# Optimization experiments

Hardware: AMD Instinct MI355X
Metric: run time of the kernel (lower is better)

Reference implementation:

```python
import jax, jax.numpy as jnp
import numpy as np

N, D, K = 32768, 256, 8192
SQRT3 = 3.0 ** 0.5


def setup_inputs() -> dict:
    key = jax.random.key(0)
    k1, k2 = jax.random.split(key)
    x = jax.random.normal(k1, (N, D), dtype=jnp.float32)
    # torch .uniform_(-sqrt(3), sqrt(3)) on an [D, K] table
    embeddings = jax.random.uniform(k2, (D, K), dtype=jnp.float32,
                                    minval=-SQRT3, maxval=SQRT3)
    return {"x": x, "embeddings": embeddings}


def reference(x, embeddings):
    # x: [N, D] (forward flattens from dim 1; 2D input is identity)
    # embeddings: [D, K]
    # squared L2 distances: ||y||^2 - 2 y.E + ||e||^2  -> [N, K]
    dist = (jnp.sum(x * x, axis=1, keepdims=True)
            - 2.0 * (x @ embeddings)
            + jnp.sum(embeddings * embeddings, axis=0, keepdims=True))
    idx = jnp.argmin(dist, axis=1)  # [N]
    # one_hot(idx) @ E^T == gather of columns of E (same math, no dense one-hot)
    quantized = jnp.take(embeddings, idx, axis=1).T  # [N, D]
    return quantized.reshape(x.shape)
```

## Files before the change

kernel.cpp:

```cpp
#include <hip/hip_runtime.h>
#include <math.h>
#include <float.h>

#define N_ROWS 32768
#define D_DIM  256
#define K_DIM  8192

#define EPS1 0.25f
#define EPS2 0.02f
#define T2CAP 4096
#define NSPLIT2 32
#define T3CAP 512
#define NSPLIT3 16

typedef _Float16 f16;
typedef _Float16 f16x8 __attribute__((ext_vector_type(8)));
typedef float f32x4 __attribute__((ext_vector_type(4)));
typedef unsigned long long u64;

#define KSPLIT 8
#define COLS_PER_SPLIT (K_DIM / KSPLIT)
#define CHUNK_COLS 32
#define NCHUNK (COLS_PER_SPLIT / CHUNK_COLS)
#define CHUNK_BYTES (CHUNK_COLS * D_DIM * 2)

#define NB_CONV 4096
#define NB_PREPE 512
#define NB_NHEN 32

typedef unsigned int u32;
typedef const u32 __attribute__((address_space(1)))* gas1_u32;
typedef u32 __attribute__((address_space(3)))* las3_u32;
__device__ __forceinline__ void gload_lds16(const void* g, void* l) {
    __builtin_amdgcn_global_load_lds((gas1_u32)g, (las3_u32)l, 16, 0, 0);
}

__global__ void prep_kernel(const float* __restrict__ X, const float* __restrict__ E,
                            f16* __restrict__ X16, float* __restrict__ ET,
                            f16* __restrict__ Epack, float* __restrict__ nhen,
                            int* __restrict__ count, int* __restrict__ count3) {
    __shared__ float t[64][65];
    const int bid = blockIdx.x;
    if (bid < NB_CONV) {
        if (bid == 0 && threadIdx.x == 0) { *count = 0; *count3 = 0; }
        const size_t i = ((size_t)bid * 256 + threadIdx.x) * 8;
        float4 a = *reinterpret_cast<const float4*>(X + i);
        float4 b = *reinterpret_cast<const float4*>(X + i + 4);
        f16x8 o;
        o[0]=(f16)a.x; o[1]=(f16)a.y; o[2]=(f16)a.z; o[3]=(f16)a.w;
        o[4]=(f16)b.x; o[5]=(f16)b.y; o[6]=(f16)b.z; o[7]=(f16)b.w;
        *reinterpret_cast<f16x8*>(X16 + i) = o;
    } else if (bid < NB_CONV + NB_PREPE) {
        const int pb = bid - NB_CONV;
        const int bk = pb & (K_DIM / 64 - 1);
        const int bd = pb >> 7;
        const int c  = threadIdx.x & 63;
        const int r0 = (threadIdx.x >> 6) * 16;
        const int d0 = bd * 64, k0 = bk * 64;
#pragma unroll
        for (int i = 0; i < 16; ++i)
            t[r0 + i][c] = E[(size_t)(d0 + r0 + i) * K_DIM + k0 + c];
        __syncthreads();
#pragma unroll
        for (int i = 0; i < 16; ++i)
            ET[(size_t)(k0 + r0 + i) * D_DIM + d0 + c] = t[c][r0 + i];
#pragma unroll
        for (int o = 0; o < 2; ++o) {
            const int out = threadIdx.x + o * 256;
            const int i16 = out >> 7;
            const int th  = (out >> 6) & 1;
            const int l   = out & 63;
            const int tile = bk * 4 + i16;
            const int tg   = bd * 2 + th;
            f16x8 frag;
#pragma unroll
            for (int j = 0; j < 8; ++j)
                frag[j] = (f16)t[32*th + (l >> 4) * 8 + j][16*i16 + (l & 15)];
            *reinterpret_cast<f16x8*>(Epack + ((size_t)(tile*8 + tg) * 512 + l * 8)) = frag;
        }
    } else {
        const int k = (bid - NB_CONV - NB_PREPE) * 256 + threadIdx.x;
        float s = 0.0f;
#pragma unroll 8
        for (int d = 0; d < D_DIM; ++d) {
            float v = E[(size_t)d * K_DIM + k];
            s = fmaf(v, v, s);
        }
        nhen[k] = -0.5f * s;
    }
}

__global__ void convx_kernel(const float* __restrict__ X, f16* __restrict__ X16,
                             int* __restrict__ count, int* __restrict__ count3) {
    if (blockIdx.x == 0 && threadIdx.x == 0) { *count = 0; *count3 = 0; }
    const size_t i = ((size_t)blockIdx.x * 256 + threadIdx.x) * 8;
    float4 a = *reinterpret_cast<const float4*>(X + i);
    float4 b = *reinterpret_cast<const float4*>(X + i + 4);
    f16x8 o;
    o[0]=(f16)a.x; o[1]=(f16)a.y; o[2]=(f16)a.z; o[3]=(f16)a.w;
    o[4]=(f16)b.x; o[5]=(f16)b.y; o[6]=(f16)b.z; o[7]=(f16)b.w;
    *reinterpret_cast<f16x8*>(X16 + i) = o;
}

__global__ void packe_kernel(const float* __restrict__ E, f16* __restrict__ Epack) {
    const int gid = blockIdx.x * 256 + threadIdx.x;
    const int l    = gid & 63;
    const int t    = (gid >> 6) & 7;
    const int tile = gid >> 9;
    const int k  = 16 * tile + (l & 15);
    const int d0 = 32 * t + (l >> 4) * 8;
    f16x8 o;
#pragma unroll
    for (int j = 0; j < 8; ++j) o[j] = (f16)E[(size_t)(d0 + j) * K_DIM + k];
    *reinterpret_cast<f16x8*>(Epack + (size_t)gid * 8) = o;
}

__global__ void nhen_kernel(const float* __restrict__ E, float* __restrict__ nhen) {
    const int k = blockIdx.x * 256 + threadIdx.x;
    float s = 0.0f;
#pragma unroll 8
    for (int d = 0; d < D_DIM; ++d) {
        float v = E[(size_t)d * K_DIM + k];
        s = fmaf(v, v, s);
    }
    nhen[k] = -0.5f * s;
}

__launch_bounds__(256, 2)
__global__ void pass1_kernel(const f16* __restrict__ X16,
                             const f16* __restrict__ Epack,
                             const float* __restrict__ nhen,
                             float* __restrict__ p_best,
                             float* __restrict__ p_sec,
                             int*   __restrict__ p_idx) {
    __shared__ f16 B_lds[3][CHUNK_BYTES / 2];
    __shared__ float nh_lds[COLS_PER_SPLIT];

    const int tid = threadIdx.x;
    const int wv = tid >> 6;
    const int lane = tid & 63;
    const int l15 = lane & 15;
    const int l4  = lane >> 4;
    const int rg = blockIdx.x >> 3;
    const int ks = blockIdx.x & 7;
    const int rowW = rg * 256 + wv * 64;
    const int colBase = ks * COLS_PER_SPLIT;

    f16x8 A[4][8];
#pragma unroll
    for (int rt = 0; rt < 4; ++rt)
#pragma unroll
        for (int t = 0; t < 8; ++t)
            A[rt][t] = *reinterpret_cast<const f16x8*>(
                X16 + (size_t)(rowW + 16*rt + l15) * D_DIM + 32*t + l4*8);

    *reinterpret_cast<float4*>(&nh_lds[tid * 4]) =
        *reinterpret_cast<const float4*>(nhen + colBase + tid * 4);

    float best[16], sec[16];
    int bbase[16];
#pragma unroll
    for (int s = 0; s < 16; ++s) { best[s] = -INFINITY; sec[s] = -INFINITY; bbase[s] = 0; }

    const char* splitSrc = (const char*)Epack + (size_t)colBase * 512;

    auto STAGE = [&](int buf, int ci) {
        const char* csrc = splitSrc + (size_t)ci * CHUNK_BYTES;
        char* cdst = (char*)&B_lds[buf][0];
#pragma unroll
        for (int c = 0; c < 4; ++c) {
            const int seg = wv * 4 + c;
            gload_lds16(csrc + seg * 1024 + (lane << 4), cdst + seg * 1024);
        }
    };

    f32x4 accA[4], accB[4];
    int cA = 0, cB = 0;

    auto TILE = [&](const f16* bufc, int ct, int nhoff,
                    f32x4 (&accN)[4], f32x4 (&accP)[4], int cP, bool doScore) {
        const float nh = nh_lds[nhoff + l15];
        const f32x4 nh4 = {nh, nh, nh, nh};
#pragma unroll
        for (int t = 0; t < 8; ++t) {
            f16x8 B = *reinterpret_cast<const f16x8*>(bufc + (ct*8 + t)*512 + lane*8);
            if (t == 0) {
#pragma unroll
                for (int rt = 0; rt < 4; ++rt)
                    accN[rt] = __builtin_amdgcn_mfma_f32_16x16x32_f16(A[rt][0], B, nh4, 0, 0, 0);
            } else {
#pragma unroll
                for (int rt = 0; rt < 4; ++rt)
                    accN[rt] = __builtin_amdgcn_mfma_f32_16x16x32_f16(A[rt][t], B, accN[rt], 0, 0, 0);
            }
            if (doScore) {
#pragma unroll
                for (int s = 2*t; s <= 2*t + 1; ++s) {
                    const int rt2 = s >> 2, r2 = s & 3;
                    const float v = accP[rt2][r2];
                    sec[s] = __builtin_amdgcn_fmed3f(v, best[s], sec[s]);
                    const bool gt = v > best[s];
                    best[s] = gt ? v : best[s];
                    bbase[s] = gt ? cP : bbase[s];
                }
            }
        }
    };

    STAGE(0, 0);
    STAGE(1, 1);
    asm volatile("s_waitcnt lgkmcnt(0)" ::: "memory");

    int cur = 0;
    for (int ci = 0; ci < NCHUNK; ++ci) {
        if (ci < NCHUNK - 1) {
            asm volatile("s_waitcnt vmcnt(4)" ::: "memory");
        } else {
            asm volatile("s_waitcnt vmcnt(0)" ::: "memory");
        }
        __builtin_amdgcn_s_barrier();
        if (ci + 2 < NCHUNK) {
            int nb = cur + 2; if (nb >= 3) nb -= 3;
            STAGE(nb, ci + 2);
        }
        const f16* bufc = &B_lds[cur][0];
        const int base = colBase + ci * CHUNK_COLS;
        if (ci == 0) {
            TILE(bufc, 0, ci*32,      accA, accB, cB, false); cA = base;
            TILE(bufc, 1, ci*32 + 16, accB, accA, cA, true);  cB = base + 16;
        } else {
            TILE(bufc, 0, ci*32,      accA, accB, cB, true);  cA = base;
            TILE(bufc, 1, ci*32 + 16, accB, accA, cA, true);  cB = base + 16;
        }
        cur = (cur + 1 == 3) ? 0 : cur + 1;
    }
#pragma unroll
    for (int s = 0; s < 16; ++s) {
        const int rt2 = s >> 2, r2 = s & 3;
        const float v = accB[rt2][r2];
        sec[s] = __builtin_amdgcn_fmed3f(v, best[s], sec[s]);
        const bool gt = v > best[s];
        best[s] = gt ? v : best[s];
        bbase[s] = gt ? cB : bbase[s];
    }

#pragma unroll
    for (int s = 0; s < 16; ++s) {
        float b = best[s], sc = sec[s];
        int k = bbase[s] + l15;
#pragma unroll
        for (int off = 8; off >= 1; off >>= 1) {
            float ob = __shfl_xor(b, off, 16);
            float os = __shfl_xor(sc, off, 16);
            int   ok = __shfl_xor(k, off, 16);
            float sm = fmaxf(fmaxf(sc, os), fminf(b, ob));
            bool take = (ob > b) || (ob == b && ok < k);
            b = take ? ob : b;
            k = take ? ok : k;
            sc = sm;
        }
        if (l15 == 0) {
            const int row = rowW + 16*(s >> 2) + 4*l4 + (s & 3);
            p_best[ks * N_ROWS + row] = b;
            p_sec [ks * N_ROWS + row] = sc;
            p_idx [ks * N_ROWS + row] = k;
        }
    }
}

__global__ void merge_kernel(const float* __restrict__ p_best,
                             const float* __restrict__ p_sec,
                             const int*   __restrict__ p_idx,
                             int* __restrict__ idxf,
                             int* __restrict__ list, int* __restrict__ count) {
    const int n = blockIdx.x * 256 + threadIdx.x;
    float b = p_best[n], sc = p_sec[n];
    int k = p_idx[n];
#pragma unroll
    for (int s = 1; s < KSPLIT; ++s) {
        float ob = p_best[s * N_ROWS + n];
        float os = p_sec [s * N_ROWS + n];
        int   ok = p_idx [s * N_ROWS + n];
        float sm = fmaxf(fmaxf(sc, os), fminf(b, ob));
        bool take = ob > b;
        b = take ? ob : b; k = take ? ok : k; sc = sm;
    }
    idxf[n] = k;
    if (2.0f * (b - sc) < EPS1) {
        int pos = atomicAdd(count, 1);
        if (pos < T2CAP) list[pos] = n;
    }
}

__launch_bounds__(256, 2)
__global__ void tier2_kernel(const float* __restrict__ X,
                             const float* __restrict__ E,
                             const float* __restrict__ nhen,
                             const int* __restrict__ list,
                             const int* __restrict__ count,
                             float* __restrict__ t2b, float* __restrict__ t2s,
                             int* __restrict__ t2i) {
    const int g  = blockIdx.x >> 5;
    const int sp = blockIdx.x & 31;
    const int cnt = min(*count, T2CAP);
    if (g * 64 >= cnt) return;

    __shared__ float xT[D_DIM][64];
    __shared__ float es[64][64];
    const int tid = threadIdx.x;
    const int tx = tid & 15, ty = tid >> 4;

    {
        const int r = tid >> 2;
        const int slot = min(g * 64 + r, cnt - 1);
        const int row = list[slot];
        const int d0 = (tid & 3) * 64;
        const float* xp = X + (size_t)row * D_DIM + d0;
#pragma unroll
        for (int i = 0; i < 64; i += 4) {
            float4 v = *reinterpret_cast<const float4*>(xp + i);
            xT[d0+i+0][r] = v.x; xT[d0+i+1][r] = v.y;
            xT[d0+i+2][r] = v.z; xT[d0+i+3][r] = v.w;
        }
    }

    float best[4], sec[4]; int bidx[4];
#pragma unroll
    for (int i = 0; i < 4; ++i) { best[i] = -INFINITY; sec[i] = -INFINITY; bidx[i] = 0; }

    const int colBase = sp * 256;
    for (int kc = 0; kc < 256; kc += 64) {
        float acc[4][4];
#pragma unroll
        for (int i = 0; i < 4; ++i)
#pragma unroll
            for (int j = 0; j < 4; ++j) acc[i][j] = 0.0f;

        for (int dc = 0; dc < D_DIM; dc += 64) {
            __syncthreads();
#pragma unroll
            for (int dd = 0; dd < 64; dd += 16) {
                int d = dd + (tid >> 4);
                float4 v = *reinterpret_cast<const float4*>(
                    &E[(size_t)(dc + d) * K_DIM + colBase + kc + (tid & 15) * 4]);
                *reinterpret_cast<float4*>(&es[d][(tid & 15) * 4]) = v;
            }
            __syncthreads();
#pragma unroll 8
            for (int d = 0; d < 64; ++d) {
                float4 xv = *reinterpret_cast<const float4*>(&xT[dc + d][ty * 4]);
                float4 ev = *reinterpret_cast<const float4*>(&es[d][tx * 4]);
                float xr[4] = {xv.x, xv.y, xv.z, xv.w};
                float ec[4] = {ev.x, ev.y, ev.z, ev.w};
#pragma unroll
                for (int i = 0; i < 4; ++i)
#pragma unroll
                    for (int j = 0; j < 4; ++j)
                        acc[i][j] = fmaf(xr[i], ec[j], acc[i][j]);
            }
        }
        float4 nhv = *reinterpret_cast<const float4*>(&nhen[colBase + kc + tx * 4]);
        float nh[4] = {nhv.x, nhv.y, nhv.z, nhv.w};
#pragma unroll
        for (int j = 0; j < 4; ++j) {
            const int k = colBase + kc + tx * 4 + j;
#pragma unroll
            for (int i = 0; i < 4; ++i) {
                float u = nh[j] + acc[i][j];
                bool gt = u > best[i];
                sec[i]  = fmaxf(sec[i], fminf(u, best[i]));
                best[i] = gt ? u : best[i];
                bidx[i] = gt ? k : bidx[i];
            }
        }
    }

#pragma unroll
    for (int off = 8; off >= 1; off >>= 1) {
#pragma unroll
        for (int i = 0; i < 4; ++i) {
            float ob = __shfl_xor(best[i], off, 16);
            float os = __shfl_xor(sec[i], off, 16);
            int   ok = __shfl_xor(bidx[i], off, 16);
            float sm = fmaxf(fmaxf(sec[i], os), fminf(best[i], ob));
            bool take = (ob > best[i]) || (ob == best[i] && ok < bidx[i]);
            best[i] = take ? ob : best[i];
            bidx[i] = take ? ok : bidx[i];
            sec[i] = sm;
        }
    }
    if (tx == 0) {
#pragma unroll
        for (int i = 0; i < 4; ++i) {
            const int slot = g * 64 + ty * 4 + i;
            if (slot < cnt) {
                t2b[sp * T2CAP + slot] = best[i];
                t2s[sp * T2CAP + slot] = sec[i];
                t2i[sp * T2CAP + slot] = bidx[i];
            }
        }
    }
}

__global__ void merge2_kernel(const float* __restrict__ t2b,
                              const float* __restrict__ t2s,
                              const int*   __restrict__ t2i,
                              const int* __restrict__ list,
                              const int* __restrict__ count,
                              int* __restrict__ idxf,
                              int* __restrict__ list3, int* __restrict__ count3,
                              u64* __restrict__ t3min) {
    const int slot = blockIdx.x * 256 + threadIdx.x;
    const int cnt = min(*count, T2CAP);
    if (slot >= cnt) return;
    float b = t2b[slot], sc = t2s[slot];
    int k = t2i[slot];
#pragma unroll
    for (int sp = 1; sp < NSPLIT2; ++sp) {
        float ob = t2b[sp * T2CAP + slot];
        float os = t2s[sp * T2CAP + slot];
        int   ok = t2i[sp * T2CAP + slot];
        float sm = fmaxf(fmaxf(sc, os), fminf(b, ob));
        bool take = ob > b;
        b = take ? ob : b; k = take ? ok : k; sc = sm;
    }
    const int n = list[slot];
    if (2.0f * (b - sc) < EPS2) {
        int pos = atomicAdd(count3, 1);
        if (pos < T3CAP) {
            list3[pos] = n;
            t3min[pos] = ~0ull;
            idxf[n] = -(pos + 1);
            return;
        }
    }
    idxf[n] = k;
}

__launch_bounds__(256)
__global__ void tier3_kernel(const float* __restrict__ X,
                             const float* __restrict__ E,
                             const int* __restrict__ list3,
                             const int* __restrict__ count3,
                             u64* __restrict__ t3min) {
    const int slot = blockIdx.x >> 4;
    const int sp   = blockIdx.x & 15;
    const int cnt = min(*count3, T3CAP);
    if (slot >= cnt) return;
    const int n = list3[slot];

    __shared__ float xs[D_DIM];
    const int tid = threadIdx.x;
    xs[tid] = X[(size_t)n * D_DIM + tid];
    __syncthreads();

    const int colBase = sp * 512;
    double best = DBL_MAX;
    int bi = 0x7fffffff;
#pragma unroll
    for (int kk = 0; kk < 512; kk += 256) {
        const int k = colBase + kk + tid;
        double s0 = 0.0, s1 = 0.0, s2 = 0.0, s3 = 0.0;
#pragma unroll 4
        for (int d = 0; d < D_DIM; d += 4) {
            double f0 = (double)xs[d+0] - (double)E[(size_t)(d+0) * K_DIM + k];
            double f1 = (double)xs[d+1] - (double)E[(size_t)(d+1) * K_DIM + k];
            double f2 = (double)xs[d+2] - (double)E[(size_t)(d+2) * K_DIM + k];
            double f3 = (double)xs[d+3] - (double)E[(size_t)(d+3) * K_DIM + k];
            s0 = fma(f0, f0, s0); s1 = fma(f1, f1, s1);
            s2 = fma(f2, f2, s2); s3 = fma(f3, f3, s3);
        }
        double s = (s0 + s1) + (s2 + s3);
        if (s < best || (s == best && k < bi)) { best = s; bi = k; }
    }

    __shared__ double bv[256];
    __shared__ int bix[256];
    bv[tid] = best; bix[tid] = bi;
    __syncthreads();
    if (tid == 0) {
        double b = bv[0]; int ix = bix[0];
        for (int t = 1; t < 256; ++t)
            if (bv[t] < b || (bv[t] == b && bix[t] < ix)) { b = bv[t]; ix = bix[t]; }
        u64 key = ((u64)__double_as_longlong(b) & ~0x1FFFull) | (u64)(unsigned)ix;
        atomicMin(&t3min[slot], key);
    }
}

__global__ void gather2_kernel(const float* __restrict__ ET,
                               const int* __restrict__ idx,
                               const u64* __restrict__ t3min,
                               float* __restrict__ out) {
    const int n  = blockIdx.x * 4 + (threadIdx.x >> 6);
    const int d4 = (threadIdx.x & 63) * 4;
    int k  = idx[n];
    if (k < 0) k = (int)(t3min[-k - 1] & 0x1FFFull);
    *reinterpret_cast<float4*>(&out[(size_t)n * D_DIM + d4]) =
        *reinterpret_cast<const float4*>(&ET[(size_t)k * D_DIM + d4]);
}

__global__ void gather_kernel(const float* __restrict__ E,
                              const int* __restrict__ idx,
                              const u64* __restrict__ t3min,
                              float* __restrict__ out) {
    const int n = blockIdx.x;
    const int d = threadIdx.x;
    int k = idx[n];
    if (k < 0) k = (int)(t3min[-k - 1] & 0x1FFFull);
    out[(size_t)n * D_DIM + d] = E[(size_t)d * K_DIM + k];
}

__global__ void fb_enorm_kernel(const float* __restrict__ E, float* __restrict__ enorm) {
    int k = blockIdx.x * 256 + threadIdx.x;
    float s = 0.0f;
#pragma unroll 8
    for (int d = 0; d < D_DIM; ++d) { float v = E[(size_t)d * K_DIM + k]; s = fmaf(v, v, s); }
    enorm[k] = s;
}

__launch_bounds__(256, 2)
__global__ void fb_dist_kernel(const float* __restrict__ X, const float* __restrict__ E,
                               const float* __restrict__ enorm,
                               int* __restrict__ idx_out, float* __restrict__ gap_out) {
    __shared__ float xT[D_DIM][64];
    __shared__ float es[64][64];
    const int tid = threadIdx.x;
    const int tx = tid & 15, ty = tid >> 4;
    const int rowBase = blockIdx.x * 64;
    {
        const int r = tid >> 2;
        const int d0 = (tid & 3) * 64;
        const float* xp = X + (size_t)(rowBase + r) * D_DIM + d0;
#pragma unroll
        for (int i = 0; i < 64; i += 4) {
            float4 v = *reinterpret_cast<const float4*>(xp + i);
            xT[d0+i+0][r]=v.x; xT[d0+i+1][r]=v.y; xT[d0+i+2][r]=v.z; xT[d0+i+3][r]=v.w;
        }
    }
    float bestVal[4], secVal[4]; int bestIdx[4];
#pragma unroll
    for (int i = 0; i < 4; ++i) { bestVal[i]=INFINITY; secVal[i]=INFINITY; bestIdx[i]=0; }
    for (int kc = 0; kc < K_DIM; kc += 64) {
        float acc[4][4];
#pragma unroll
        for (int i=0;i<4;++i)
#pragma unroll
            for (int j=0;j<4;++j) acc[i][j]=0.f;
        for (int dc = 0; dc < D_DIM; dc += 64) {
            __syncthreads();
#pragma unroll
            for (int dd = 0; dd < 64; dd += 16) {
                int d = dd + (tid >> 4);
                float4 v = *reinterpret_cast<const float4*>(
                    &E[(size_t)(dc+d)*K_DIM + kc + (tid&15)*4]);
                *reinterpret_cast<float4*>(&es[d][(tid&15)*4]) = v;
            }
            __syncthreads();
#pragma unroll 8
            for (int d = 0; d < 64; ++d) {
                float4 xv = *reinterpret_cast<const float4*>(&xT[dc+d][ty*4]);
                float4 ev = *reinterpret_cast<const float4*>(&es[d][tx*4]);
                float xr[4]={xv.x,xv.y,xv.z,xv.w}, ec[4]={ev.x,ev.y,ev.z,ev.w};
#pragma unroll
                for (int i=0;i<4;++i)
#pragma unroll
                    for (int j=0;j<4;++j) acc[i][j]=fmaf(xr[i],ec[j],acc[i][j]);
            }
        }
        float4 env = *reinterpret_cast<const float4*>(&enorm[kc + tx*4]);
        float en[4]={env.x,env.y,env.z,env.w};
#pragma unroll
        for (int j=0;j<4;++j) {
            int k = kc + tx*4 + j;
#pragma unroll
            for (int i=0;i<4;++i) {
                float s = fmaf(-2.0f, acc[i][j], en[j]);
                if (s < bestVal[i]) { secVal[i]=bestVal[i]; bestVal[i]=s; bestIdx[i]=k; }
                else if (s < secVal[i]) secVal[i]=s;
            }
        }
    }
#pragma unroll
    for (int off=8; off>=1; off>>=1) {
#pragma unroll
        for (int i=0;i<4;++i) {
            float oB=__shfl_xor(bestVal[i],off,16);
            int oI=__shfl_xor(bestIdx[i],off,16);
            float oS=__shfl_xor(secVal[i],off,16);
            float ms=fminf(fminf(secVal[i],oS),fmaxf(bestVal[i],oB));
            if (oB<bestVal[i] || (oB==bestVal[i] && oI<bestIdx[i])) { bestVal[i]=oB; bestIdx[i]=oI; }
            secVal[i]=ms;
        }
    }
    if (tx==0) {
#pragma unroll
        for (int i=0;i<4;++i) {
            idx_out[rowBase + ty*4 + i] = bestIdx[i];
            gap_out[rowBase + ty*4 + i] = secVal[i]-bestVal[i];
        }
    }
}

__launch_bounds__(256)
__global__ void fb_refine_kernel(const float* __restrict__ X, const float* __restrict__ E,
                                 const float* __restrict__ gap, int* __restrict__ idx) {
    const int n = blockIdx.x;
    if (gap[n] >= 0.0625f) return;
    __shared__ float xs[D_DIM];
    const int tid = threadIdx.x;
    xs[tid] = X[(size_t)n * D_DIM + tid];
    __syncthreads();
    double best = DBL_MAX; int bi = 0x7fffffff;
    for (int k = tid; k < K_DIM; k += 256) {
        double s0=0,s1=0,s2=0,s3=0;
#pragma unroll 4
        for (int d = 0; d < D_DIM; d += 4) {
            double f0=(double)xs[d+0]-(double)E[(size_t)(d+0)*K_DIM+k];
            double f1=(double)xs[d+1]-(double)E[(size_t)(d+1)*K_DIM+k];
            double f2=(double)xs[d+2]-(double)E[(size_t)(d+2)*K_DIM+k];
            double f3=(double)xs[d+3]-(double)E[(size_t)(d+3)*K_DIM+k];
            s0=fma(f0,f0,s0); s1=fma(f1,f1,s1); s2=fma(f2,f2,s2); s3=fma(f3,f3,s3);
        }
        double s=(s0+s1)+(s2+s3);
        if (s<best){best=s;bi=k;}
    }
    __shared__ double bv[256]; __shared__ int bix[256];
    bv[tid]=best; bix[tid]=bi;
    __syncthreads();
    if (tid==0) {
        double b=bv[0]; int ix=bix[0];
        for (int t=1;t<256;++t)
            if (bv[t]<b || (bv[t]==b && bix[t]<ix)) { b=bv[t]; ix=bix[t]; }
        idx[n]=ix;
    }
}

__global__ void fb_gather_kernel(const float* __restrict__ E,
                                 const int* __restrict__ idx,
                                 float* __restrict__ out) {
    const int n = blockIdx.x;
    const int d = threadIdx.x;
    const int k = idx[n];
    out[(size_t)n * D_DIM + d] = E[(size_t)d * K_DIM + k];
}

extern "C" void kernel_launch(void* const* d_in, const int* in_sizes, int n_in,
                              void* d_out, int out_size, void* d_ws, size_t ws_size,
                              hipStream_t stream) {
    const float* X = (const float*)d_in[0];
    const float* E = (const float*)d_in[1];
    float* out = (float*)d_out;
    char* ws = (char*)d_ws;

    const size_t o_nhen  = 0;
    const size_t o_pb    = 32768;
    const size_t o_ps    = o_pb  + (size_t)KSPLIT * N_ROWS * 4;
    const size_t o_pi    = o_ps  + (size_t)KSPLIT * N_ROWS * 4;
    const size_t o_idx   = o_pi  + (size_t)KSPLIT * N_ROWS * 4;
    const size_t o_list  = o_idx + (size_t)N_ROWS * 4;
    const size_t o_count = o_list + (size_t)T2CAP * 4;
    const size_t o_t2b   = o_count + 256;
    const size_t o_t2s   = o_t2b + (size_t)NSPLIT2 * T2CAP * 4;
    const size_t o_t2i   = o_t2s + (size_t)NSPLIT2 * T2CAP * 4;
    const size_t o_list3 = o_t2i + (size_t)NSPLIT2 * T2CAP * 4;
    const size_t o_t3min = o_list3 + (size_t)T3CAP * 4;
    const size_t o_x16   = o_t3min + (size_t)T3CAP * 8;
    const size_t o_epack = o_x16 + (size_t)N_ROWS * D_DIM * 2;
    const size_t NEED_BASE = o_epack + (size_t)D_DIM * K_DIM * 2;
    const size_t o_et    = NEED_BASE;
    const size_t NEED_FULL = o_et + (size_t)D_DIM * K_DIM * 4;

    if (ws_size >= NEED_BASE) {
        float*  nhen  = (float*) (ws + o_nhen);
        float*  p_b   = (float*) (ws + o_pb);
        float*  p_s   = (float*) (ws + o_ps);
        int*    p_i   = (int*)   (ws + o_pi);
        int*    idxf  = (int*)   (ws + o_idx);
        int*    list  = (int*)   (ws + o_list);
        int*    count = (int*)   (ws + o_count);
        int*    count3= (int*)   (ws + o_count + 4);
        float*  t2b   = (float*) (ws + o_t2b);
        float*  t2s   = (float*) (ws + o_t2s);
        int*    t2i   = (int*)   (ws + o_t2i);
        int*    list3 = (int*)   (ws + o_list3);
        u64*    t3min = (u64*)   (ws + o_t3min);
        f16*    X16   = (f16*)   (ws + o_x16);
        f16*    Epack = (f16*)   (ws + o_epack);
        float*  ET    = (float*) (ws + o_et);
        const bool haveET = ws_size >= NEED_FULL;

        if (haveET) {
            prep_kernel<<<NB_CONV + NB_PREPE + NB_NHEN, 256, 0, stream>>>(
                X, E, X16, ET, Epack, nhen, count, count3);
        } else {
            convx_kernel<<<NB_CONV, 256, 0, stream>>>(X, X16, count, count3);
            packe_kernel<<<(K_DIM / 16) * 8 * 64 / 256, 256, 0, stream>>>(E, Epack);
            nhen_kernel<<<NB_NHEN, 256, 0, stream>>>(E, nhen);
        }
        pass1_kernel<<<(N_ROWS / 256) * KSPLIT, 256, 0, stream>>>(
            X16, Epack, nhen, p_b, p_s, p_i);
        merge_kernel<<<N_ROWS / 256, 256, 0, stream>>>(
            p_b, p_s, p_i, idxf, list, count);
        tier2_kernel<<<(T2CAP / 64) * NSPLIT2, 256, 0, stream>>>(
            X, E, nhen, list, count, t2b, t2s, t2i);
        merge2_kernel<<<T2CAP / 256, 256, 0, stream>>>(
            t2b, t2s, t2i, list, count, idxf, list3, count3, t3min);
        tier3_kernel<<<T3CAP * NSPLIT3, 256, 0, stream>>>(
            X, E, list3, count3, t3min);
        if (haveET)
            gather2_kernel<<<N_ROWS / 4, 256, 0, stream>>>(ET, idxf, t3min, out);
        else
            gather_kernel<<<N_ROWS, 256, 0, stream>>>(E, idxf, t3min, out);
    } else {
        float* enorm = (float*)ws;
        int*   idx   = (int*)(ws + 32768);
        float* gap   = (float*)(ws + 32768 + (size_t)N_ROWS * 4);
        fb_enorm_kernel<<<K_DIM / 256, 256, 0, stream>>>(E, enorm);
        fb_dist_kernel<<<N_ROWS / 64, 256, 0, stream>>>(X, E, enorm, idx, gap);
        fb_refine_kernel<<<N_ROWS, 256, 0, stream>>>(X, E, gap, idx);
        fb_gather_kernel<<<N_ROWS, 256, 0, stream>>>(E, idx, out);
    }
}
```

Baseline: 300.5 us.

## Fuse merge, refine tiers and gather into one cooperative persistent kernel

Replaces the five post-pass1 launches (merge, tier2, merge2, tier3, gather) with a single cooperative kernel of 512 persistent blocks that uses grid-wide syncs between phases and grid-strides over the data-dependent tier work. The aim is to remove per-launch overhead and the fixed grids that launch mostly idle blocks when candidate counts are small. In exchange, grid.sync costs are added, parallelism is capped at 512 blocks for the gather and tier phases, and the code depends on cooperative launch succeeding, falling back to the old launches otherwise.

Measured after the change: 562.7 us. 1.87x slower.

```diff
diff --git a/kernel.cpp b/kernel.cpp
--- a/kernel.cpp
+++ b/kernel.cpp
@@ -1,6 +1,9 @@
 #include <hip/hip_runtime.h>
+#include <hip/hip_cooperative_groups.h>
 #include <math.h>
 #include <float.h>
+
+namespace cg = cooperative_groups;
 
 #define N_ROWS 32768
 #define D_DIM  256
@@ -27,6 +30,8 @@
 #define NB_CONV 4096
 #define NB_PREPE 512
 #define NB_NHEN 32
+
+#define CLEAN_BLOCKS 512
 
 typedef unsigned int u32;
 typedef const u32 __attribute__((address_space(1)))* gas1_u32;
@@ -268,6 +273,237 @@
     }
 }
 
+__launch_bounds__(256, 2)
+__global__ void cleanup_kernel(const float* __restrict__ X,
+                               const float* __restrict__ E,
+                               const float* __restrict__ ET,
+                               const float* __restrict__ nhen,
+                               const float* __restrict__ p_b,
+                               const float* __restrict__ p_s,
+                               const int*   __restrict__ p_i,
+                               int* __restrict__ idxf,
+                               int* __restrict__ list,
+                               int* __restrict__ count,
+                               float* __restrict__ t2b,
+                               float* __restrict__ t2s,
+                               int* __restrict__ t2i,
+                               int* __restrict__ list3,
+                               int* __restrict__ count3,
+                               u64* __restrict__ t3min,
+                               float* __restrict__ out) {
+    cg::grid_group grid = cg::this_grid();
+    __shared__ float xT[D_DIM][64];
+    __shared__ float es[64][64];
+    const int tid = threadIdx.x;
+    const int bid = blockIdx.x;
+
+    {
+        const int n = bid * 256 + tid;
+        if (n < N_ROWS) {
+            float b = p_b[n], sc = p_s[n];
+            int k = p_i[n];
+#pragma unroll
+            for (int s = 1; s < KSPLIT; ++s) {
+                float ob = p_b[s * N_ROWS + n];
+                float os = p_s[s * N_ROWS + n];
+                int   ok = p_i[s * N_ROWS + n];
+                float sm = fmaxf(fmaxf(sc, os), fminf(b, ob));
+                bool take = ob > b;
+                b = take ? ob : b; k = take ? ok : k; sc = sm;
+            }
+            idxf[n] = k;
+            if (2.0f * (b - sc) < EPS1) {
+                int pos = atomicAdd(count, 1);
+                if (pos < T2CAP) list[pos] = n;
+            }
+        }
+    }
+    grid.sync();
+
+    const int cnt = min(*(volatile int*)count, T2CAP);
+    const int ngroups = (cnt + 63) >> 6;
+    for (int task = bid; task < ngroups * NSPLIT2; task += CLEAN_BLOCKS) {
+        __syncthreads();
+        const int g  = task >> 5;
+        const int sp = task & 31;
+        const int tx = tid & 15, ty = tid >> 4;
+        {
+            const int r = tid >> 2;
+            const int slot = min(g * 64 + r, cnt - 1);
+            const int row = list[slot];
+            const int d0 = (tid & 3) * 64;
+            const float* xp = X + (size_t)row * D_DIM + d0;
+#pragma unroll
+            for (int i = 0; i < 64; i += 4) {
+                float4 v = *reinterpret_cast<const float4*>(xp + i);
+                xT[d0+i+0][r] = v.x; xT[d0+i+1][r] = v.y;
+                xT[d0+i+2][r] = v.z; xT[d0+i+3][r] = v.w;
+            }
+        }
+        float best[4], sec[4]; int bidx[4];
+#pragma unroll
+        for (int i = 0; i < 4; ++i) { best[i] = -INFINITY; sec[i] = -INFINITY; bidx[i] = 0; }
+
+        const int colBase = sp * 256;
+        for (int kc = 0; kc < 256; kc += 64) {
+            float acc[4][4];
+#pragma unroll
+            for (int i = 0; i < 4; ++i)
+#pragma unroll
+                for (int j = 0; j < 4; ++j) acc[i][j] = 0.0f;
+
+            for (int dc = 0; dc < D_DIM; dc += 64) {
+                __syncthreads();
+#pragma unroll
+                for (int dd = 0; dd < 64; dd += 16) {
+                    int d = dd + (tid >> 4);
+                    float4 v = *reinterpret_cast<const float4*>(
+                        &E[(size_t)(dc + d) * K_DIM + colBase + kc + (tid & 15) * 4]);
+                    *reinterpret_cast<float4*>(&es[d][(tid & 15) * 4]) = v;
+                }
+                __syncthreads();
+#pragma unroll 8
+                for (int d = 0; d < 64; ++d) {
+                    float4 xv = *reinterpret_cast<const float4*>(&xT[dc + d][ty * 4]);
+                    float4 ev = *reinterpret_cast<const float4*>(&es[d][tx * 4]);
+                    float xr[4] = {xv.x, xv.y, xv.z, xv.w};
+                    float ec[4] = {ev.x, ev.y, ev.z, ev.w};
+#pragma unroll
+                    for (int i = 0; i < 4; ++i)
+#pragma unroll
+                        for (int j = 0; j < 4; ++j)
+                            acc[i][j] = fmaf(xr[i], ec[j], acc[i][j]);
+                }
+            }
+            float4 nhv = *reinterpret_cast<const float4*>(&nhen[colBase + kc + tx * 4]);
+            float nh[4] = {nhv.x, nhv.y, nhv.z, nhv.w};
+#pragma unroll
+            for (int j = 0; j < 4; ++j) {
+                const int k = colBase + kc + tx * 4 + j;
+#pragma unroll
+                for (int i = 0; i < 4; ++i) {
+                    float u = nh[j] + acc[i][j];
+                    bool gt = u > best[i];
+                    sec[i]  = fmaxf(sec[i], fminf(u, best[i]));
+                    best[i] = gt ? u : best[i];
+                    bidx[i] = gt ? k : bidx[i];
+                }
+            }
+        }
+
+#pragma unroll
+        for (int off = 8; off >= 1; off >>= 1) {
+#pragma unroll
+            for (int i = 0; i < 4; ++i) {
+                float ob = __shfl_xor(best[i], off, 16);
+                float os = __shfl_xor(sec[i], off, 16);
+                int   ok = __shfl_xor(bidx[i], off, 16);
+                float sm = fmaxf(fmaxf(sec[i], os), fminf(best[i], ob));
+                bool take = (ob > best[i]) || (ob == best[i] && ok < bidx[i]);
+                best[i] = take ? ob : best[i];
+                bidx[i] = take ? ok : bidx[i];
+                sec[i] = sm;
+            }
+        }
+        if (tx == 0) {
+#pragma unroll
+            for (int i = 0; i < 4; ++i) {
+                const int slot = g * 64 + ty * 4 + i;
+                if (slot < cnt) {
+                    t2b[sp * T2CAP + slot] = best[i];
+                    t2s[sp * T2CAP + slot] = sec[i];
+                    t2i[sp * T2CAP + slot] = bidx[i];
+                }
+            }
+        }
+    }
+    grid.sync();
+
+    {
+        const int slot = bid * 256 + tid;
+        if (slot < cnt) {
+            float b = t2b[slot], sc = t2s[slot];
+            int k = t2i[slot];
+#pragma unroll
+            for (int sp = 1; sp < NSPLIT2; ++sp) {
+                float ob = t2b[sp * T2CAP + slot];
+                float os = t2s[sp * T2CAP + slot];
+                int   ok = t2i[sp * T2CAP + slot];
+                float sm = fmaxf(fmaxf(sc, os), fminf(b, ob));
+                bool take = ob > b;
+                b = take ? ob : b; k = take ? ok : k; sc = sm;
+            }
+            const int n = list[slot];
+            bool t3 = false;
+            if (2.0f * (b - sc) < EPS2) {
+                int pos = atomicAdd(count3, 1);
+                if (pos < T3CAP) {
+                    list3[pos] = n;
+                    t3min[pos] = ~0ull;
+                    idxf[n] = -(pos + 1);
+                    t3 = true;
+                }
+            }
+            if (!t3) idxf[n] = k;
+        }
+    }
+    grid.sync();
+
+    const int cnt3 = min(*(volatile int*)count3, T3CAP);
+    {
+        float*  xs  = &es[0][0];
+        double* bv  = (double*)&es[4][0];
+        int*    bix = (int*)&es[12][0];
+        for (int task = bid; task < cnt3 * NSPLIT3; task += CLEAN_BLOCKS) {
+            __syncthreads();
+            const int slot = task >> 4;
+            const int sp   = task & 15;
+            const int n = list3[slot];
+            xs[tid] = X[(size_t)n * D_DIM + tid];
+            __syncthreads();
+
+            const int colBase = sp * 512;
+            double best = DBL_MAX;
+            int bi = 0x7fffffff;
+#pragma unroll
+            for (int kk = 0; kk < 512; kk += 256) {
+                const int k = colBase + kk + tid;
+                double s0 = 0.0, s1 = 0.0, s2 = 0.0, s3 = 0.0;
+#pragma unroll 4
+                for (int d = 0; d < D_DIM; d += 4) {
+                    double f0 = (double)xs[d+0] - (double)E[(size_t)(d+0) * K_DIM + k];
+                    double f1 = (double)xs[d+1] - (double)E[(size_t)(d+1) * K_DIM + k];
+                    double f2 = (double)xs[d+2] - (double)E[(size_t)(d+2) * K_DIM + k];
+                    double f3 = (double)xs[d+3] - (double)E[(size_t)(d+3) * K_DIM + k];
+                    s0 = fma(f0, f0, s0); s1 = fma(f1, f1, s1);
+                    s2 = fma(f2, f2, s2); s3 = fma(f3, f3, s3);
+                }
+                double s = (s0 + s1) + (s2 + s3);
+                if (s < best || (s == best && k < bi)) { best = s; bi = k; }
+            }
+            bv[tid] = best; bix[tid] = bi;
+            __syncthreads();
+            if (tid == 0) {
+                double b = bv[0]; int ix = bix[0];
+                for (int t = 1; t < 256; ++t)
+                    if (bv[t] < b || (bv[t] == b && bix[t] < ix)) { b = bv[t]; ix = bix[t]; }
+                u64 key = ((u64)__double_as_longlong(b) & ~0x1FFFull) | (u64)(unsigned)ix;
+                atomicMin(&t3min[slot], key);
+            }
+        }
+    }
+    grid.sync();
+
+    for (int i = bid * 256 + tid; i < N_ROWS * 64; i += CLEAN_BLOCKS * 256) {
+        const int n  = i >> 6;
+        const int d4 = (i & 63) * 4;
+        int k = idxf[n];
+        if (k < 0) k = (int)(t3min[-k - 1] & 0x1FFFull);
+        *reinterpret_cast<float4*>(&out[(size_t)n * D_DIM + d4]) =
+            *reinterpret_cast<const float4*>(&ET[(size_t)k * D_DIM + d4]);
+    }
+}
+
 __global__ void merge_kernel(const float* __restrict__ p_best,
                              const float* __restrict__ p_sec,
                              const int*   __restrict__ p_idx,
@@ -699,18 +935,34 @@
         }
         pass1_kernel<<<(N_ROWS / 256) * KSPLIT, 256, 0, stream>>>(
             X16, Epack, nhen, p_b, p_s, p_i);
-        merge_kernel<<<N_ROWS / 256, 256, 0, stream>>>(
-            p_b, p_s, p_i, idxf, list, count);
-        tier2_kernel<<<(T2CAP / 64) * NSPLIT2, 256, 0, stream>>>(
-            X, E, nhen, list, count, t2b, t2s, t2i);
-        merge2_kernel<<<T2CAP / 256, 256, 0, stream>>>(
-            t2b, t2s, t2i, list, count, idxf, list3, count3, t3min);
-        tier3_kernel<<<T3CAP * NSPLIT3, 256, 0, stream>>>(
-            X, E, list3, count3, t3min);
-        if (haveET)
-            gather2_kernel<<<N_ROWS / 4, 256, 0, stream>>>(ET, idxf, t3min, out);
-        else
-            gather_kernel<<<N_ROWS, 256, 0, stream>>>(E, idxf, t3min, out);
+
+        bool coopOK = false;
+        if (haveET) {
+            void* args[] = {(void*)&X, (void*)&E, (void*)&ET, (void*)&nhen,
+                            (void*)&p_b, (void*)&p_s, (void*)&p_i,
+                            (void*)&idxf, (void*)&list, (void*)&count,
+                            (void*)&t2b, (void*)&t2s, (void*)&t2i,
+                            (void*)&list3, (void*)&count3, (void*)&t3min,
+                            (void*)&out};
+            hipError_t err = hipLaunchCooperativeKernel(
+                (const void*)cleanup_kernel, dim3(CLEAN_BLOCKS), dim3(256),
+                args, 0, stream);
+            coopOK = (err == hipSuccess);
+        }
+        if (!coopOK) {
+            merge_kernel<<<N_ROWS / 256, 256, 0, stream>>>(
+                p_b, p_s, p_i, idxf, list, count);
+            tier2_kernel<<<(T2CAP / 64) * NSPLIT2, 256, 0, stream>>>(
+                X, E, nhen, list, count, t2b, t2s, t2i);
+            merge2_kernel<<<T2CAP / 256, 256, 0, stream>>>(
+                t2b, t2s, t2i, list, count, idxf, list3, count3, t3min);
+            tier3_kernel<<<T3CAP * NSPLIT3, 256, 0, stream>>>(
+                X, E, list3, count3, t3min);
+            if (haveET)
+                gather2_kernel<<<N_ROWS / 4, 256, 0, stream>>>(ET, idxf, t3min, out);
+            else
+                gather_kernel<<<N_ROWS, 256, 0, stream>>>(E, idxf, t3min, out);
+        }
     } else {
         float* enorm = (float*)ws;
         int*   idx   = (int*)(ws + 32768);
```
